# Kernel tuning notes

Hardware: AMD Instinct MI355X
Metric: run time of the kernel (lower is better)

Reference implementation:

```python
import jax, jax.numpy as jnp
from jax import lax
import numpy as np

B, N = 16, 4096
NPOINT, RADIUS, NSAMPLE = 1024, 0.2, 32
IN_CH = 64
MLP = [64, 64, 128]
EPS = 1e-5  # torch BatchNorm2d default


def setup_inputs() -> dict:
    key = jax.random.key(0)
    ks = jax.random.split(key, 2 + 2 * len(MLP))
    inp = {
        "xyz": jax.random.uniform(ks[0], (B, 3, N), jnp.float32),
        "points": jax.random.normal(ks[1], (B, IN_CH, N), jnp.float32),
    }
    last = IN_CH + 3
    for i, out in enumerate(MLP):
        inp[f"W{i}"] = jax.random.normal(ks[2 + 2 * i], (last, out), jnp.float32) / np.float32(np.sqrt(last))
        inp[f"b{i}"] = jnp.zeros((out,), jnp.float32)
        inp[f"g{i}"] = jnp.ones((out,), jnp.float32)
        inp[f"be{i}"] = jnp.zeros((out,), jnp.float32)
        last = out
    return inp


def _fps(x):
    """Farthest point sampling. x: [B,N,3] -> [B,NPOINT] int32 (start idx 0)."""
    Bv, Nn, _ = x.shape

    def step(carry, _):
        dist, far = carry
        c = jnp.take_along_axis(x, far[:, None, None], axis=1)  # [B,1,3]
        d = jnp.sum((x - c) ** 2, axis=-1)                      # [B,N]
        dist = jnp.minimum(dist, d)
        return (dist, jnp.argmax(dist, axis=-1).astype(jnp.int32)), far

    init = (jnp.full((Bv, Nn), 1e10, x.dtype), jnp.zeros((Bv,), jnp.int32))
    _, cent = lax.scan(step, init, None, length=NPOINT)
    return cent.T  # [B, NPOINT]


def _ball_query(x, new_xyz):
    """x: [B,N,3], new_xyz: [B,S,3] -> idx [B,S,NSAMPLE] int32."""
    Nn = x.shape[1]
    sqr = jnp.sum((new_xyz[:, :, None, :] - x[:, None, :, :]) ** 2, axis=-1)  # [B,S,N]
    idx = jnp.where(sqr > RADIUS ** 2, Nn, jnp.arange(Nn, dtype=jnp.int32))
    idx = jnp.sort(idx, axis=-1)[:, :, :NSAMPLE]  # first NSAMPLE in-radius indices
    first = idx[:, :, :1]
    return jnp.where(idx == Nn, first, idx)


def _gather(pts, idx):
    """pts: [B,N,C], idx: [B,S,K] -> [B,S,K,C]."""
    Bv, S, K = idx.shape
    flat = idx.reshape(Bv, S * K)
    return jnp.take_along_axis(pts, flat[:, :, None], axis=1).reshape(Bv, S, K, pts.shape[-1])


def _forward(xyz, points, params):
    x = xyz.transpose(0, 2, 1)      # [B,N,3]
    p = points.transpose(0, 2, 1)   # [B,N,D]
    fps_idx = _fps(x)
    new_xyz = jnp.take_along_axis(x, fps_idx[:, :, None], axis=1)  # [B,S,3]
    idx = _ball_query(x, new_xyz)
    g_xyz = _gather(x, idx) - new_xyz[:, :, None, :]               # [B,S,K,3]
    feats = jnp.concatenate([g_xyz, _gather(p, idx)], axis=-1)     # [B,S,K,3+D]
    for (W, b, g, be) in params:
        feats = jnp.einsum('bskc,cd->bskd', feats, W) + b          # 1x1 conv
        mean = feats.mean(axis=(0, 1, 2))                          # BN train-mode batch stats
        var = feats.var(axis=(0, 1, 2))
        feats = jax.nn.relu(g * (feats - mean) * lax.rsqrt(var + EPS) + be)
    new_points = feats.max(axis=2).transpose(0, 2, 1)              # max over nsample -> [B,C',S]
    return new_xyz.transpose(0, 2, 1), new_points


def reference(xyz, points, W0, b0, g0, be0, W1, b1, g1, be1, W2, b2, g2, be2):
    params = [(W0, b0, g0, be0), (W1, b1, g1, be1), (W2, b2, g2, be2)]
    return _forward(xyz, points, params)
```

## Files before the change

### kernel.cpp

```cpp
#include <hip/hip_runtime.h>
#include <hip/hip_bf16.h>
#include <cstdint>


typedef __attribute__((ext_vector_type(8))) short bf16x8;
typedef __attribute__((ext_vector_type(4))) float f32x4;

#define LDA 104

__device__ __forceinline__ unsigned short f2bf(float f) {
  unsigned x = __float_as_uint(f);
  unsigned r = (x + 0x7FFFu + ((x >> 16) & 1u)) >> 16;
  return (unsigned short)r;
}
__device__ __forceinline__ float bf2f(unsigned short u) {
  return __uint_as_float(((unsigned)u) << 16);
}

template <int CTRL>
__device__ __forceinline__ unsigned long long dppmax(unsigned long long k) {
  int lo = (int)(unsigned)k;
  int hi = (int)(unsigned)(k >> 32);
  int plo = __builtin_amdgcn_update_dpp(lo, lo, CTRL, 0xF, 0xF, false);
  int phi = __builtin_amdgcn_update_dpp(hi, hi, CTRL, 0xF, 0xF, false);
  unsigned long long o =
      ((unsigned long long)(unsigned)phi << 32) | (unsigned)plo;
  return (o > k) ? o : k;
}

__global__ __attribute__((amdgpu_flat_work_group_size(256, 256),
                          amdgpu_waves_per_eu(1, 1)))
void fps_prep_kernel(
    const float* __restrict__ xyz, const float* __restrict__ points,
    const float* __restrict__ W0, const float* __restrict__ W1,
    const float* __restrict__ W2, unsigned short* __restrict__ pT,
    unsigned short* __restrict__ w0t, unsigned short* __restrict__ w1t,
    unsigned short* __restrict__ w2t, float* __restrict__ stats_all,
    float* __restrict__ out, float4* __restrict__ centers4)
{
  __shared__ __align__(16) char smraw[61568];
  int tid = threadIdx.x;
  if (blockIdx.x >= 16) {
    int pb = blockIdx.x - 16;
    if (pb < 1024) {
      float (*tile)[65] = (float (*)[65])smraw;
      int b = pb >> 6;
      int n0 = (pb & 63) << 6;
      const float* pbp = points + ((size_t)b << 18);
      for (int i = tid; i < 4096; i += 256) {
        int cc = i >> 6, nn = i & 63;
        tile[cc][nn] = pbp[((size_t)cc << 12) + n0 + nn];
      }
      __syncthreads();
      for (int i = tid; i < 4096; i += 256) {
        int nn = i >> 6, cc = i & 63;
        pT[(((size_t)((b << 12) + n0 + nn)) << 6) + cc] = f2bf(tile[cc][nn]);
      }
    } else {
      for (int i = tid; i < 27136; i += 256) {
        if (i < 6656) {
          int nn = i / 104, kk = i % 104;
          float v = (kk < 64) ? W0[(3 + kk) * 64 + nn]
                              : ((kk < 67) ? W0[(kk - 64) * 64 + nn] : 0.f);
          w0t[i] = f2bf(v);
        } else if (i < 13312) {
          int j = i - 6656; int nn = j / 104, kk = j % 104;
          float v = (kk < 64) ? W1[kk * 64 + nn] : 0.f;
          w1t[j] = f2bf(v);
        } else if (i < 26624) {
          int j = i - 13312; int nn = j / 104, kk = j % 104;
          float v = (kk < 64) ? W2[kk * 128 + nn] : 0.f;
          w2t[j] = f2bf(v);
        } else {
          stats_all[i - 26624] = 0.f;
        }
      }
    }
    return;
  }
  float* xs  = (float*)smraw;
  float* ys  = xs + 4096;
  float* zs  = ys + 4096;
  float* cxl = zs + 4096;
  float* cyl = cxl + 1024;
  float* czl = cyl + 1024;
  unsigned long long (*keybuf)[4] =
      (unsigned long long (*)[4])(smraw + 61440);

  int b = blockIdx.x;
  const float* xb = xyz + (size_t)b * 12288;
  float px[16], py[16], pz[16], dist[16];
#pragma unroll
  for (int j = 0; j < 16; ++j) {
    int n = tid + (j << 8);
    px[j] = xb[n]; py[j] = xb[4096 + n]; pz[j] = xb[8192 + n];
    xs[n] = px[j]; ys[n] = py[j]; zs[n] = pz[j];
    dist[j] = 1e10f;
  }
  __syncthreads();
  float cx = xs[0], cy = ys[0], cz = zs[0];
  if (tid == 0) { cxl[0] = cx; cyl[0] = cy; czl[0] = cz; }
  int w = tid >> 6;
  int lane = tid & 63;
  for (int it = 1; it < 1024; ++it) {
    float bv = -1.f; int bi = 0;
#pragma unroll
    for (int j = 0; j < 16; ++j) {
      float dx = __fsub_rn(px[j], cx);
      float dy = __fsub_rn(py[j], cy);
      float dz = __fsub_rn(pz[j], cz);
      float d  = __fadd_rn(__fadd_rn(__fmul_rn(dx, dx), __fmul_rn(dy, dy)),
                           __fmul_rn(dz, dz));
      float nd = fminf(dist[j], d);
      dist[j] = nd;
      if (nd > bv) { bv = nd; bi = tid + (j << 8); }
    }
    unsigned long long k =
        ((unsigned long long)__float_as_uint(bv) << 32) | (unsigned)(~bi);
    k = dppmax<0xB1>(k);
    k = dppmax<0x4E>(k);
    k = dppmax<0x141>(k);
    k = dppmax<0x140>(k);
    k = dppmax<0x142>(k);
    k = dppmax<0x143>(k);
    int p = it & 1;
    if (lane == 63) keybuf[p][w] = k;
    __syncthreads();
    uint4 ka2 = *(const uint4*)&keybuf[p][0];
    uint4 kb2 = *(const uint4*)&keybuf[p][2];
    unsigned long long k0 = ((unsigned long long)ka2.y << 32) | ka2.x;
    unsigned long long k1 = ((unsigned long long)ka2.w << 32) | ka2.z;
    unsigned long long k2 = ((unsigned long long)kb2.y << 32) | kb2.x;
    unsigned long long k3 = ((unsigned long long)kb2.w << 32) | kb2.z;
    unsigned long long m01 = (k1 > k0) ? k1 : k0;
    unsigned long long m23 = (k3 > k2) ? k3 : k2;
    unsigned long long km  = (m23 > m01) ? m23 : m01;
    int gi = (int)(~(unsigned)km) & 4095;
    cx = xs[gi]; cy = ys[gi]; cz = zs[gi];
    if (tid == 0) { cxl[it] = cx; cyl[it] = cy; czl[it] = cz; }
  }
  __syncthreads();
  for (int it = tid; it < 1024; it += 256) {
    float x = cxl[it], y = cyl[it], z = czl[it];
    out[b * 3072 + it]        = x;
    out[b * 3072 + 1024 + it] = y;
    out[b * 3072 + 2048 + it] = z;
    centers4[(b << 10) + it]  = make_float4(x, y, z, 0.f);
  }
}

__global__ __launch_bounds__(256) void ball_kernel(const float* __restrict__ xyz,
                                                   const float4* __restrict__ centers4,
                                                   int* __restrict__ ballidx)
{
  __shared__ float xs[4096], ys[4096], zs[4096];
  int tid = threadIdx.x;
  int b = blockIdx.x >> 4;
  int g = blockIdx.x & 15;
  const float* xb = xyz + (size_t)b * 12288;
  for (int i = tid; i < 4096; i += 256) {
    xs[i] = xb[i]; ys[i] = xb[4096 + i]; zs[i] = xb[8192 + i];
  }
  __syncthreads();
  int w = tid >> 6, lane = tid & 63;
  unsigned long long lmask = (1ull << lane) - 1ull;
  for (int j = 0; j < 16; ++j) {
    int s = (g << 6) + (j << 2) + w;
    float4 c = centers4[(b << 10) + s];
    int* ob = ballidx + (((size_t)((b << 10) + s)) << 5);
    int cnt = 0, first = 0;
    for (int m = 0; m < 64; ++m) {
      int n = (m << 6) + lane;
      float dx = __fsub_rn(xs[n], c.x);
      float dy = __fsub_rn(ys[n], c.y);
      float dz = __fsub_rn(zs[n], c.z);
      float d  = __fadd_rn(__fadd_rn(__fmul_rn(dx, dx), __fmul_rn(dy, dy)),
                           __fmul_rn(dz, dz));
      bool hit = !(d > 0.04f);
      unsigned long long mask = __ballot(hit);
      if (cnt == 0 && mask != 0ull)
        first = (m << 6) + (__ffsll((long long)mask) - 1);
      int p = cnt + (int)__popcll(mask & lmask);
      if (hit && p < 32) ob[p] = n;
      cnt += (int)__popcll(mask);
      if (cnt >= 32) break;
    }
    if (lane < 32 && lane >= cnt) ob[lane] = first;
  }
}

__global__ __launch_bounds__(256) void gemm1_kernel(
    const float* __restrict__ xyz, const unsigned short* __restrict__ pT,
    const unsigned short* __restrict__ w0t, const float* __restrict__ b0,
    const float4* __restrict__ centers4, const int* __restrict__ ballidx,
    unsigned short* __restrict__ feats1, float* __restrict__ partials)
{
  __shared__ unsigned short As[64 * LDA];
  __shared__ unsigned short Wt[64 * LDA];
  __shared__ float red[2][4][64];
  int tid = threadIdx.x;
  int blockbase = blockIdx.x << 8;
  int b = blockbase >> 15;
  {
    const uint4* wsrc = (const uint4*)w0t;
    uint4* wdst = (uint4*)Wt;
    for (int i = tid; i < 832; i += 256) wdst[i] = wsrc[i];
  }
  int lane = tid & 63, w = tid >> 6;
  int mrow = (w << 4) + (lane & 15);
  int quad = lane >> 4;
  float a0acc = 0.f, a1acc = 0.f;
  for (int t = 0; t < 4; ++t) {
    int rowbase = blockbase + (t << 6);
    {
      int rl = tid >> 2, part = tid & 3;
      int r = rowbase + rl;
      int n = ballidx[r];
      const uint4* psrc = (const uint4*)(pT + (((size_t)((b << 12) + n)) << 6));
      uint4* adst = (uint4*)(As + rl * LDA);
      adst[part * 2]     = psrc[part * 2];
      adst[part * 2 + 1] = psrc[part * 2 + 1];
      adst[8 + part] = make_uint4(0, 0, 0, 0);
      if (part == 0) {
        int ci = r >> 5;
        float4 c = centers4[ci];
        unsigned short* arow = As + rl * LDA;
        arow[64] = f2bf(__fsub_rn(xyz[(size_t)b * 12288 + n],        c.x));
        arow[65] = f2bf(__fsub_rn(xyz[(size_t)b * 12288 + 4096 + n], c.y));
        arow[66] = f2bf(__fsub_rn(xyz[(size_t)b * 12288 + 8192 + n], c.z));
      }
    }
    __syncthreads();
    f32x4 acc[4];
#pragma unroll
    for (int nt = 0; nt < 4; ++nt) acc[nt] = (f32x4){0.f, 0.f, 0.f, 0.f};
#pragma unroll
    for (int kt = 0; kt < 3; ++kt) {
      int ko = kt * 32 + (quad << 3);
      bf16x8 a = *(const bf16x8*)(As + mrow * LDA + ko);
#pragma unroll
      for (int nt = 0; nt < 4; ++nt) {
        bf16x8 bb = *(const bf16x8*)(Wt + ((nt << 4) + (lane & 15)) * LDA + ko);
        acc[nt] = __builtin_amdgcn_mfma_f32_16x16x32_bf16(a, bb, acc[nt], 0, 0, 0);
      }
    }
#pragma unroll
    for (int nt = 0; nt < 4; ++nt) {
      int cch = (nt << 4) + (lane & 15);
      float bias = b0[cch];
      float ssum = 0.f, sq = 0.f;
#pragma unroll
      for (int r2 = 0; r2 < 4; ++r2) {
        float y = acc[nt][r2] + bias;
        int ml = (w << 4) + (quad << 2) + r2;
        feats1[(((size_t)(rowbase + ml)) << 6) + cch] = f2bf(y);
        ssum += y; sq += y * y;
      }
      ssum += __shfl_xor(ssum, 16); ssum += __shfl_xor(ssum, 32);
      sq   += __shfl_xor(sq, 16);   sq   += __shfl_xor(sq, 32);
      if (quad == 0) { red[0][w][cch] = ssum; red[1][w][cch] = sq; }
    }
    __syncthreads();
    if (tid < 64) {
      a0acc += red[0][0][tid] + red[0][1][tid] + red[0][2][tid] + red[0][3][tid];
      a1acc += red[1][0][tid] + red[1][1][tid] + red[1][2][tid] + red[1][3][tid];
    }
  }
  if (tid < 64) {
    partials[(size_t)blockIdx.x * 256 + tid]      = a0acc;
    partials[(size_t)blockIdx.x * 256 + 64 + tid] = a1acc;
  }
}

__global__ __launch_bounds__(256) void gemm2_kernel(
    const unsigned short* __restrict__ featsIn, const unsigned short* __restrict__ wt,
    const float* __restrict__ bias_g, const float* __restrict__ ss_in,
    unsigned short* __restrict__ featsOut, float* __restrict__ partials)
{
  __shared__ unsigned short As[64 * LDA];
  __shared__ unsigned short Wt[64 * LDA];
  __shared__ float red[2][4][64];
  __shared__ float ssl[128];
  int tid = threadIdx.x;
  int blockbase = blockIdx.x << 8;
  if (tid < 128) ssl[tid] = ss_in[tid];
  {
    const uint4* wsrc = (const uint4*)wt;
    uint4* wdst = (uint4*)Wt;
    for (int i = tid; i < 832; i += 256) wdst[i] = wsrc[i];
  }
  int lane = tid & 63, w = tid >> 6;
  int mrow = (w << 4) + (lane & 15);
  int quad = lane >> 4;
  float a0acc = 0.f, a1acc = 0.f;
  __syncthreads();
  for (int t = 0; t < 4; ++t) {
    int rowbase = blockbase + (t << 6);
    {
      int rl = tid >> 2, part = tid & 3;
      size_t r = (size_t)rowbase + rl;
      union { uint4 v[2]; unsigned short u[16]; } tt;
      const uint4* src = (const uint4*)(featsIn + (r << 6));
      tt.v[0] = src[part * 2]; tt.v[1] = src[part * 2 + 1];
      union { uint4 v[2]; unsigned short u[16]; } o;
#pragma unroll
      for (int e = 0; e < 16; ++e) {
        int cch = (part << 4) + e;
        float f = bf2f(tt.u[e]);
        float y = fmaxf(f * ssl[cch] + ssl[64 + cch], 0.f);
        o.u[e] = f2bf(y);
      }
      uint4* adst = (uint4*)(As + rl * LDA + (part << 4));
      adst[0] = o.v[0]; adst[1] = o.v[1];
    }
    __syncthreads();
    f32x4 acc[4];
#pragma unroll
    for (int nt = 0; nt < 4; ++nt) acc[nt] = (f32x4){0.f, 0.f, 0.f, 0.f};
#pragma unroll
    for (int kt = 0; kt < 2; ++kt) {
      int ko = kt * 32 + (quad << 3);
      bf16x8 a = *(const bf16x8*)(As + mrow * LDA + ko);
#pragma unroll
      for (int nt = 0; nt < 4; ++nt) {
        bf16x8 bb = *(const bf16x8*)(Wt + ((nt << 4) + (lane & 15)) * LDA + ko);
        acc[nt] = __builtin_amdgcn_mfma_f32_16x16x32_bf16(a, bb, acc[nt], 0, 0, 0);
      }
    }
#pragma unroll
    for (int nt = 0; nt < 4; ++nt) {
      int cch = (nt << 4) + (lane & 15);
      float bias = bias_g[cch];
      float ssum = 0.f, sq = 0.f;
#pragma unroll
      for (int r2 = 0; r2 < 4; ++r2) {
        float y = acc[nt][r2] + bias;
        int ml = (w << 4) + (quad << 2) + r2;
        featsOut[(((size_t)(rowbase + ml)) << 6) + cch] = f2bf(y);
        ssum += y; sq += y * y;
      }
      ssum += __shfl_xor(ssum, 16); ssum += __shfl_xor(ssum, 32);
      sq   += __shfl_xor(sq, 16);   sq   += __shfl_xor(sq, 32);
      if (quad == 0) { red[0][w][cch] = ssum; red[1][w][cch] = sq; }
    }
    __syncthreads();
    if (tid < 64) {
      a0acc += red[0][0][tid] + red[0][1][tid] + red[0][2][tid] + red[0][3][tid];
      a1acc += red[1][0][tid] + red[1][1][tid] + red[1][2][tid] + red[1][3][tid];
    }
  }
  if (tid < 64) {
    partials[(size_t)blockIdx.x * 256 + tid]      = a0acc;
    partials[(size_t)blockIdx.x * 256 + 64 + tid] = a1acc;
  }
}

__global__ __launch_bounds__(256) void gemm3_stats_kernel(
    const unsigned short* __restrict__ feats2, const unsigned short* __restrict__ w2t,
    const float* __restrict__ b2, const float* __restrict__ ss2,
    float* __restrict__ partials, float* __restrict__ y3mx,
    float* __restrict__ y3mn)
{
  __shared__ unsigned short As[64 * LDA];
  __shared__ unsigned short Wt[128 * LDA];
  __shared__ float red[2][4][128];
  __shared__ float mxw[4][128];
  __shared__ float mnw[4][128];
  __shared__ float ssl[128];
  int tid = threadIdx.x;
  int blockbase = blockIdx.x << 8;
  if (tid < 128) ssl[tid] = ss2[tid];
  {
    const uint4* wsrc = (const uint4*)w2t;
    uint4* wdst = (uint4*)Wt;
    for (int i = tid; i < 1664; i += 256) wdst[i] = wsrc[i];
  }
  int lane = tid & 63, w = tid >> 6;
  int mrow = (w << 4) + (lane & 15);
  int quad = lane >> 4;
  float a0acc = 0.f, a1acc = 0.f;
  __syncthreads();
  for (int t = 0; t < 4; ++t) {
    int rowbase = blockbase + (t << 6);
    {
      int rl = tid >> 2, part = tid & 3;
      size_t r = (size_t)rowbase + rl;
      union { uint4 v[2]; unsigned short u[16]; } tt;
      const uint4* src = (const uint4*)(feats2 + (r << 6));
      tt.v[0] = src[part * 2]; tt.v[1] = src[part * 2 + 1];
      union { uint4 v[2]; unsigned short u[16]; } o;
#pragma unroll
      for (int e = 0; e < 16; ++e) {
        int cch = (part << 4) + e;
        float f = bf2f(tt.u[e]);
        float y = fmaxf(f * ssl[cch] + ssl[64 + cch], 0.f);
        o.u[e] = f2bf(y);
      }
      uint4* adst = (uint4*)(As + rl * LDA + (part << 4));
      adst[0] = o.v[0]; adst[1] = o.v[1];
    }
    __syncthreads();
    f32x4 acc[8];
#pragma unroll
    for (int nt = 0; nt < 8; ++nt) acc[nt] = (f32x4){0.f, 0.f, 0.f, 0.f};
#pragma unroll
    for (int kt = 0; kt < 2; ++kt) {
      int ko = kt * 32 + (quad << 3);
      bf16x8 a = *(const bf16x8*)(As + mrow * LDA + ko);
#pragma unroll
      for (int nt = 0; nt < 8; ++nt) {
        bf16x8 bb = *(const bf16x8*)(Wt + ((nt << 4) + (lane & 15)) * LDA + ko);
        acc[nt] = __builtin_amdgcn_mfma_f32_16x16x32_bf16(a, bb, acc[nt], 0, 0, 0);
      }
    }
#pragma unroll
    for (int nt = 0; nt < 8; ++nt) {
      int cch = (nt << 4) + (lane & 15);
      float bias = b2[cch];
      float ssum = 0.f, sq = 0.f;
      float mx = -3.4e38f, mn = 3.4e38f;
#pragma unroll
      for (int r2 = 0; r2 < 4; ++r2) {
        float y = acc[nt][r2] + bias;
        ssum += y; sq += y * y;
        mx = fmaxf(mx, y); mn = fminf(mn, y);
      }
      ssum += __shfl_xor(ssum, 16); ssum += __shfl_xor(ssum, 32);
      sq   += __shfl_xor(sq, 16);   sq   += __shfl_xor(sq, 32);
      mx = fmaxf(mx, __shfl_xor(mx, 16)); mx = fmaxf(mx, __shfl_xor(mx, 32));
      mn = fminf(mn, __shfl_xor(mn, 16)); mn = fminf(mn, __shfl_xor(mn, 32));
      if (quad == 0) {
        red[0][w][cch] = ssum; red[1][w][cch] = sq;
        mxw[w][cch] = mx; mnw[w][cch] = mn;
      }
    }
    __syncthreads();
    if (tid < 128) {
      a0acc += red[0][0][tid] + red[0][1][tid] + red[0][2][tid] + red[0][3][tid];
      a1acc += red[1][0][tid] + red[1][1][tid] + red[1][2][tid] + red[1][3][tid];
    }
    {
      int c2 = tid >> 7, cch = tid & 127;
      int cg = (rowbase >> 5) + c2;
      y3mx[((size_t)cg << 7) + cch] = fmaxf(mxw[2 * c2][cch], mxw[2 * c2 + 1][cch]);
      y3mn[((size_t)cg << 7) + cch] = fminf(mnw[2 * c2][cch], mnw[2 * c2 + 1][cch]);
    }
  }
  if (tid < 128) {
    partials[(size_t)blockIdx.x * 256 + tid]       = a0acc;
    partials[(size_t)blockIdx.x * 256 + 128 + tid] = a1acc;
  }
}

__global__ __launch_bounds__(256) void reduce_kernel(const float* __restrict__ partials,
                                                     float* __restrict__ stats, int twoC)
{
  int tid = threadIdx.x;
  if (tid < twoC) {
    int row0 = blockIdx.x << 5;
    float s = 0.f;
    for (int r = 0; r < 32; ++r) s += partials[((size_t)(row0 + r)) * 256 + tid];
    atomicAdd(&stats[tid], s);
  }
}

__global__ void finalize_kernel(const float* __restrict__ stats, const float* __restrict__ g,
                                const float* __restrict__ be, float* __restrict__ ss, int C)
{
  int c = threadIdx.x;
  if (c < C) {
    const float invM = 1.f / 524288.f;
    float mean = stats[c] * invM;
    float ex2  = stats[C + c] * invM;
    float var  = ex2 - mean * mean;
    float sc   = g[c] / sqrtf(var + 1e-5f);
    ss[c]     = sc;
    ss[C + c] = be[c] - mean * sc;
  }
}

__global__ __launch_bounds__(256) void bn3_out_kernel(
    const float* __restrict__ y3mx, const float* __restrict__ y3mn,
    const float* __restrict__ ss3, float* __restrict__ out)
{
  __shared__ float t2[64][65];
  __shared__ float sl[128];
  int tid = threadIdx.x;
  int b = blockIdx.x >> 5;
  int rest = blockIdx.x & 31;
  int s0 = (rest & 15) << 6;
  int c0 = (rest >> 4) << 6;
  if (tid < 64) sl[tid] = ss3[c0 + tid];
  else if (tid < 128) sl[tid] = ss3[128 + c0 + (tid - 64)];
  __syncthreads();
  for (int i = tid; i < 4096; i += 256) {
    int row = i >> 6, col = i & 63;
    size_t cg = (size_t)((b << 10) + s0 + row);
    float mx = y3mx[(cg << 7) + c0 + col];
    float mn = y3mn[(cg << 7) + c0 + col];
    float sc = sl[col], sh = sl[64 + col];
    float ye = (sc >= 0.f) ? mx : mn;
    t2[row][col] = fmaxf(ye * sc + sh, 0.f);
  }
  __syncthreads();
  for (int i = tid; i < 4096; i += 256) {
    int crow = i >> 6, scol = i & 63;
    out[49152 + ((size_t)b << 17) + (size_t)(c0 + crow) * 1024 + s0 + scol] = t2[scol][crow];
  }
}

extern "C" void kernel_launch(void* const* d_in, const int* in_sizes, int n_in,
                              void* d_out, int out_size, void* d_ws, size_t ws_size,
                              hipStream_t stream)
{
  (void)in_sizes; (void)n_in; (void)out_size; (void)ws_size;
  const float* xyz    = (const float*)d_in[0];
  const float* points = (const float*)d_in[1];
  const float* W0  = (const float*)d_in[2];
  const float* b0  = (const float*)d_in[3];
  const float* g0  = (const float*)d_in[4];
  const float* be0 = (const float*)d_in[5];
  const float* W1  = (const float*)d_in[6];
  const float* b1  = (const float*)d_in[7];
  const float* g1  = (const float*)d_in[8];
  const float* be1 = (const float*)d_in[9];
  const float* W2  = (const float*)d_in[10];
  const float* b2  = (const float*)d_in[11];
  const float* g2  = (const float*)d_in[12];
  const float* be2 = (const float*)d_in[13];
  float* out = (float*)d_out;

  char* base = (char*)d_ws;
  size_t off = 0;
  auto alloc = [&](size_t bytes) -> void* {
    void* p = base + off;
    off += (bytes + 255) & ~(size_t)255;
    return p;
  };
  unsigned short* pT     = (unsigned short*)alloc((size_t)16 * 4096 * 64 * 2);
  unsigned short* w0t    = (unsigned short*)alloc(64 * LDA * 2);
  unsigned short* w1t    = (unsigned short*)alloc(64 * LDA * 2);
  unsigned short* w2t    = (unsigned short*)alloc(128 * LDA * 2);
  float* stats_all       = (float*)alloc(512 * 4);
  float* ss_all          = (float*)alloc(512 * 4);
  float4* centers4       = (float4*)alloc((size_t)16 * 1024 * 16);
  int* ballidx           = (int*)alloc((size_t)16 * 1024 * 32 * 4);
  unsigned short* feats1 = (unsigned short*)alloc((size_t)524288 * 64 * 2);
  unsigned short* feats2 = (unsigned short*)alloc((size_t)524288 * 64 * 2);
  float* partials        = (float*)alloc((size_t)2048 * 256 * 4);

  float* y3mx = (float*)feats1;
  float* y3mn = y3mx + (size_t)16384 * 128;

  float* stats1 = stats_all;       float* stats2 = stats_all + 128; float* stats3 = stats_all + 256;
  float* ss1 = ss_all;             float* ss2 = ss_all + 128;       float* ss3 = ss_all + 256;

  fps_prep_kernel<<<1041, 256, 0, stream>>>(xyz, points, W0, W1, W2, pT, w0t, w1t,
                                            w2t, stats_all, out, centers4);
  ball_kernel<<<256, 256, 0, stream>>>(xyz, centers4, ballidx);
  gemm1_kernel<<<2048, 256, 0, stream>>>(xyz, pT, w0t, b0, centers4, ballidx, feats1, partials);
  reduce_kernel<<<64, 256, 0, stream>>>(partials, stats1, 128);
  finalize_kernel<<<1, 64, 0, stream>>>(stats1, g0, be0, ss1, 64);
  gemm2_kernel<<<2048, 256, 0, stream>>>(feats1, w1t, b1, ss1, feats2, partials);
  reduce_kernel<<<64, 256, 0, stream>>>(partials, stats2, 128);
  finalize_kernel<<<1, 64, 0, stream>>>(stats2, g1, be1, ss2, 64);
  gemm3_stats_kernel<<<2048, 256, 0, stream>>>(feats2, w2t, b2, ss2, partials, y3mx, y3mn);
  reduce_kernel<<<64, 256, 0, stream>>>(partials, stats3, 256);
  finalize_kernel<<<1, 128, 0, stream>>>(stats3, g2, be2, ss3, 128);
  bn3_out_kernel<<<512, 256, 0, stream>>>(y3mx, y3mn, ss3, out);
}
```

Before: 914.1 us.

## Fuse FPS, prep, ball query and GEMM1 into persistent cooperative kernel

```diff
diff --git a/kernel.cpp b/kernel.cpp
--- a/kernel.cpp
+++ b/kernel.cpp
@@ -28,247 +28,291 @@
   return (o > k) ? o : k;
 }
 
+__device__ __forceinline__ void spin_ge(int* p, int need) {
+  while (__hip_atomic_load(p, __ATOMIC_ACQUIRE, __HIP_MEMORY_SCOPE_AGENT) < need)
+    __builtin_amdgcn_s_sleep(32);
+}
+
 __global__ __attribute__((amdgpu_flat_work_group_size(256, 256),
                           amdgpu_waves_per_eu(1, 1)))
-void fps_prep_kernel(
+void mega_kernel(
     const float* __restrict__ xyz, const float* __restrict__ points,
     const float* __restrict__ W0, const float* __restrict__ W1,
-    const float* __restrict__ W2, unsigned short* __restrict__ pT,
-    unsigned short* __restrict__ w0t, unsigned short* __restrict__ w1t,
-    unsigned short* __restrict__ w2t, float* __restrict__ stats_all,
-    float* __restrict__ out, float4* __restrict__ centers4)
+    const float* __restrict__ W2, const float* __restrict__ b0,
+    unsigned short* __restrict__ pT, unsigned short* __restrict__ w0t,
+    unsigned short* __restrict__ w1t, unsigned short* __restrict__ w2t,
+    float4* __restrict__ centers4, unsigned short* __restrict__ feats1,
+    float* __restrict__ partials, float* __restrict__ out,
+    int* __restrict__ ctrl)
 {
   __shared__ __align__(16) char smraw[61568];
+  __shared__ int tkt_s;
   int tid = threadIdx.x;
-  if (blockIdx.x >= 16) {
-    int pb = blockIdx.x - 16;
-    if (pb < 1024) {
-      float (*tile)[65] = (float (*)[65])smraw;
-      int b = pb >> 6;
-      int n0 = (pb & 63) << 6;
-      const float* pbp = points + ((size_t)b << 18);
-      for (int i = tid; i < 4096; i += 256) {
-        int cc = i >> 6, nn = i & 63;
-        tile[cc][nn] = pbp[((size_t)cc << 12) + n0 + nn];
-      }
+  int bx = blockIdx.x;
+  int* progress  = ctrl;
+  int* prep_done = ctrl + 16;
+  int* g1_ticket = ctrl + 17;
+
+  if (bx < 16) {
+    float* xs  = (float*)smraw;
+    float* ys  = xs + 4096;
+    float* zs  = ys + 4096;
+    float* cxl = zs + 4096;
+    float* cyl = cxl + 1024;
+    float* czl = cyl + 1024;
+    unsigned long long (*keybuf)[4] =
+        (unsigned long long (*)[4])(smraw + 61440);
+
+    int b = bx;
+    const float* xb = xyz + (size_t)b * 12288;
+    float px[16], py[16], pz[16], dist[16];
+#pragma unroll
+    for (int j = 0; j < 16; ++j) {
+      int n = tid + (j << 8);
+      px[j] = xb[n]; py[j] = xb[4096 + n]; pz[j] = xb[8192 + n];
+      xs[n] = px[j]; ys[n] = py[j]; zs[n] = pz[j];
+      dist[j] = 1e10f;
+    }
+    __syncthreads();
+    float cx = xs[0], cy = ys[0], cz = zs[0];
+    if (tid == 0) { cxl[0] = cx; cyl[0] = cy; czl[0] = cz; }
+    int w = tid >> 6;
+    int lane = tid & 63;
+    for (int it = 1; it < 1024; ++it) {
+      float bv = -1.f; int bi = 0;
+#pragma unroll
+      for (int j = 0; j < 16; ++j) {
+        float dx = __fsub_rn(px[j], cx);
+        float dy = __fsub_rn(py[j], cy);
+        float dz = __fsub_rn(pz[j], cz);
+        float d  = __fadd_rn(__fadd_rn(__fmul_rn(dx, dx), __fmul_rn(dy, dy)),
+                             __fmul_rn(dz, dz));
+        float nd = fminf(dist[j], d);
+        dist[j] = nd;
+        if (nd > bv) { bv = nd; bi = tid + (j << 8); }
+      }
+      unsigned long long k =
+          ((unsigned long long)__float_as_uint(bv) << 32) | (unsigned)(~bi);
+      k = dppmax<0xB1>(k);
+      k = dppmax<0x4E>(k);
+      k = dppmax<0x141>(k);
+      k = dppmax<0x140>(k);
+      k = dppmax<0x142>(k);
+      k = dppmax<0x143>(k);
+      int p = it & 1;
+      if (lane == 63) keybuf[p][w] = k;
       __syncthreads();
-      for (int i = tid; i < 4096; i += 256) {
-        int nn = i >> 6, cc = i & 63;
-        pT[(((size_t)((b << 12) + n0 + nn)) << 6) + cc] = f2bf(tile[cc][nn]);
-      }
-    } else {
-      for (int i = tid; i < 27136; i += 256) {
-        if (i < 6656) {
-          int nn = i / 104, kk = i % 104;
-          float v = (kk < 64) ? W0[(3 + kk) * 64 + nn]
-                              : ((kk < 67) ? W0[(kk - 64) * 64 + nn] : 0.f);
-          w0t[i] = f2bf(v);
-        } else if (i < 13312) {
-          int j = i - 6656; int nn = j / 104, kk = j % 104;
-          float v = (kk < 64) ? W1[kk * 64 + nn] : 0.f;
-          w1t[j] = f2bf(v);
-        } else if (i < 26624) {
-          int j = i - 13312; int nn = j / 104, kk = j % 104;
-          float v = (kk < 64) ? W2[kk * 128 + nn] : 0.f;
-          w2t[j] = f2bf(v);
-        } else {
-          stats_all[i - 26624] = 0.f;
-        }
-      }
-    }
-    return;
-  }
-  float* xs  = (float*)smraw;
-  float* ys  = xs + 4096;
-  float* zs  = ys + 4096;
-  float* cxl = zs + 4096;
-  float* cyl = cxl + 1024;
-  float* czl = cyl + 1024;
-  unsigned long long (*keybuf)[4] =
-      (unsigned long long (*)[4])(smraw + 61440);
-
-  int b = blockIdx.x;
-  const float* xb = xyz + (size_t)b * 12288;
-  float px[16], py[16], pz[16], dist[16];
-#pragma unroll
-  for (int j = 0; j < 16; ++j) {
-    int n = tid + (j << 8);
-    px[j] = xb[n]; py[j] = xb[4096 + n]; pz[j] = xb[8192 + n];
-    xs[n] = px[j]; ys[n] = py[j]; zs[n] = pz[j];
-    dist[j] = 1e10f;
-  }
+      uint4 ka2 = *(const uint4*)&keybuf[p][0];
+      uint4 kb2 = *(const uint4*)&keybuf[p][2];
+      unsigned long long k0 = ((unsigned long long)ka2.y << 32) | ka2.x;
+      unsigned long long k1 = ((unsigned long long)ka2.w << 32) | ka2.z;
+      unsigned long long k2 = ((unsigned long long)kb2.y << 32) | kb2.x;
+      unsigned long long k3 = ((unsigned long long)kb2.w << 32) | kb2.z;
+      unsigned long long m01 = (k1 > k0) ? k1 : k0;
+      unsigned long long m23 = (k3 > k2) ? k3 : k2;
+      unsigned long long km  = (m23 > m01) ? m23 : m01;
+      int gi = (int)(~(unsigned)km) & 4095;
+      cx = xs[gi]; cy = ys[gi]; cz = zs[gi];
+      if (tid == 0) { cxl[it] = cx; cyl[it] = cy; czl[it] = cz; }
+      if ((it & 63) == 0) {
+        int base = it - 64;
+        if (tid < 64) {
+          int s = base + tid;
+          centers4[(b << 10) + s] = make_float4(cxl[s], cyl[s], czl[s], 0.f);
+        }
+        if (tid == 0) {
+          __threadfence();
+          __hip_atomic_store(&progress[b], it, __ATOMIC_RELEASE,
+                             __HIP_MEMORY_SCOPE_AGENT);
+        }
+      }
+    }
+    __syncthreads();
+    for (int it = tid; it < 1024; it += 256) {
+      float x = cxl[it], y = cyl[it], z = czl[it];
+      out[b * 3072 + it]        = x;
+      out[b * 3072 + 1024 + it] = y;
+      out[b * 3072 + 2048 + it] = z;
+      centers4[(b << 10) + it]  = make_float4(x, y, z, 0.f);
+    }
+    __syncthreads();
+    if (tid == 0) {
+      __threadfence();
+      __hip_atomic_store(&progress[b], 1024, __ATOMIC_RELEASE,
+                         __HIP_MEMORY_SCOPE_AGENT);
+    }
+  } else {
+    int wid = bx - 16;
+    int cnt = 0;
+    for (int t = wid; t < 1025; t += 240) {
+      __syncthreads();
+      if (t < 1024) {
+        float (*tile)[65] = (float (*)[65])smraw;
+        int b = t >> 6;
+        int n0 = (t & 63) << 6;
+        const float* pbp = points + ((size_t)b << 18);
+        for (int i = tid; i < 4096; i += 256) {
+          int cc = i >> 6, nn = i & 63;
+          tile[cc][nn] = pbp[((size_t)cc << 12) + n0 + nn];
+        }
+        __syncthreads();
+        for (int i = tid; i < 4096; i += 256) {
+          int nn = i >> 6, cc = i & 63;
+          pT[(((size_t)((b << 12) + n0 + nn)) << 6) + cc] = f2bf(tile[cc][nn]);
+        }
+      } else {
+        for (int i = tid; i < 26624; i += 256) {
+          if (i < 6656) {
+            int nn = i / 104, kk = i % 104;
+            float v = (kk < 64) ? W0[(3 + kk) * 64 + nn]
+                                : ((kk < 67) ? W0[(kk - 64) * 64 + nn] : 0.f);
+            w0t[i] = f2bf(v);
+          } else if (i < 13312) {
+            int j = i - 6656; int nn = j / 104, kk = j % 104;
+            w1t[j] = f2bf((kk < 64) ? W1[kk * 64 + nn] : 0.f);
+          } else {
+            int j = i - 13312; int nn = j / 104, kk = j % 104;
+            w2t[j] = f2bf((kk < 64) ? W2[kk * 128 + nn] : 0.f);
+          }
+        }
+      }
+      ++cnt;
+    }
+    __syncthreads();
+    if (tid == 0) {
+      __threadfence();
+      __hip_atomic_fetch_add(prep_done, cnt, __ATOMIC_RELEASE,
+                             __HIP_MEMORY_SCOPE_AGENT);
+    }
+  }
+
+  spin_ge(prep_done, 1025);
   __syncthreads();
-  float cx = xs[0], cy = ys[0], cz = zs[0];
-  if (tid == 0) { cxl[0] = cx; cyl[0] = cy; czl[0] = cz; }
-  int w = tid >> 6;
-  int lane = tid & 63;
-  for (int it = 1; it < 1024; ++it) {
-    float bv = -1.f; int bi = 0;
-#pragma unroll
-    for (int j = 0; j < 16; ++j) {
-      float dx = __fsub_rn(px[j], cx);
-      float dy = __fsub_rn(py[j], cy);
-      float dz = __fsub_rn(pz[j], cz);
-      float d  = __fadd_rn(__fadd_rn(__fmul_rn(dx, dx), __fmul_rn(dy, dy)),
-                           __fmul_rn(dz, dz));
-      float nd = fminf(dist[j], d);
-      dist[j] = nd;
-      if (nd > bv) { bv = nd; bi = tid + (j << 8); }
-    }
-    unsigned long long k =
-        ((unsigned long long)__float_as_uint(bv) << 32) | (unsigned)(~bi);
-    k = dppmax<0xB1>(k);
-    k = dppmax<0x4E>(k);
-    k = dppmax<0x141>(k);
-    k = dppmax<0x140>(k);
-    k = dppmax<0x142>(k);
-    k = dppmax<0x143>(k);
-    int p = it & 1;
-    if (lane == 63) keybuf[p][w] = k;
-    __syncthreads();
-    uint4 ka2 = *(const uint4*)&keybuf[p][0];
-    uint4 kb2 = *(const uint4*)&keybuf[p][2];
-    unsigned long long k0 = ((unsigned long long)ka2.y << 32) | ka2.x;
-    unsigned long long k1 = ((unsigned long long)ka2.w << 32) | ka2.z;
-    unsigned long long k2 = ((unsigned long long)kb2.y << 32) | kb2.x;
-    unsigned long long k3 = ((unsigned long long)kb2.w << 32) | kb2.z;
-    unsigned long long m01 = (k1 > k0) ? k1 : k0;
-    unsigned long long m23 = (k3 > k2) ? k3 : k2;
-    unsigned long long km  = (m23 > m01) ? m23 : m01;
-    int gi = (int)(~(unsigned)km) & 4095;
-    cx = xs[gi]; cy = ys[gi]; cz = zs[gi];
-    if (tid == 0) { cxl[it] = cx; cyl[it] = cy; czl[it] = cz; }
-  }
-  __syncthreads();
-  for (int it = tid; it < 1024; it += 256) {
-    float x = cxl[it], y = cyl[it], z = czl[it];
-    out[b * 3072 + it]        = x;
-    out[b * 3072 + 1024 + it] = y;
-    out[b * 3072 + 2048 + it] = z;
-    centers4[(b << 10) + it]  = make_float4(x, y, z, 0.f);
-  }
-}
-
-__global__ __launch_bounds__(256) void ball_kernel(const float* __restrict__ xyz,
-                                                   const float4* __restrict__ centers4,
-                                                   int* __restrict__ ballidx)
-{
-  __shared__ float xs[4096], ys[4096], zs[4096];
-  int tid = threadIdx.x;
-  int b = blockIdx.x >> 4;
-  int g = blockIdx.x & 15;
-  const float* xb = xyz + (size_t)b * 12288;
-  for (int i = tid; i < 4096; i += 256) {
-    xs[i] = xb[i]; ys[i] = xb[4096 + i]; zs[i] = xb[8192 + i];
-  }
-  __syncthreads();
-  int w = tid >> 6, lane = tid & 63;
-  unsigned long long lmask = (1ull << lane) - 1ull;
-  for (int j = 0; j < 16; ++j) {
-    int s = (g << 6) + (j << 2) + w;
-    float4 c = centers4[(b << 10) + s];
-    int* ob = ballidx + (((size_t)((b << 10) + s)) << 5);
-    int cnt = 0, first = 0;
-    for (int m = 0; m < 64; ++m) {
-      int n = (m << 6) + lane;
-      float dx = __fsub_rn(xs[n], c.x);
-      float dy = __fsub_rn(ys[n], c.y);
-      float dz = __fsub_rn(zs[n], c.z);
-      float d  = __fadd_rn(__fadd_rn(__fmul_rn(dx, dx), __fmul_rn(dy, dy)),
-                           __fmul_rn(dz, dz));
-      bool hit = !(d > 0.04f);
-      unsigned long long mask = __ballot(hit);
-      if (cnt == 0 && mask != 0ull)
-        first = (m << 6) + (__ffsll((long long)mask) - 1);
-      int p = cnt + (int)__popcll(mask & lmask);
-      if (hit && p < 32) ob[p] = n;
-      cnt += (int)__popcll(mask);
-      if (cnt >= 32) break;
-    }
-    if (lane < 32 && lane >= cnt) ob[lane] = first;
-  }
-}
-
-__global__ __launch_bounds__(256) void gemm1_kernel(
-    const float* __restrict__ xyz, const unsigned short* __restrict__ pT,
-    const unsigned short* __restrict__ w0t, const float* __restrict__ b0,
-    const float4* __restrict__ centers4, const int* __restrict__ ballidx,
-    unsigned short* __restrict__ feats1, float* __restrict__ partials)
-{
-  __shared__ unsigned short As[64 * LDA];
-  __shared__ unsigned short Wt[64 * LDA];
-  __shared__ float red[2][4][64];
-  int tid = threadIdx.x;
-  int blockbase = blockIdx.x << 8;
-  int b = blockbase >> 15;
-  {
-    const uint4* wsrc = (const uint4*)w0t;
-    uint4* wdst = (uint4*)Wt;
-    for (int i = tid; i < 832; i += 256) wdst[i] = wsrc[i];
-  }
+
+  float* xs = (float*)smraw;
+  float* ys = xs + 4096;
+  float* zs = ys + 4096;
+  unsigned short* As = (unsigned short*)smraw;
+  unsigned short* Wt = (unsigned short*)(smraw + 13312);
+  float* red = (float*)(smraw + 26624);
+  int* idxl = (int*)(smraw + 60416);
+
   int lane = tid & 63, w = tid >> 6;
   int mrow = (w << 4) + (lane & 15);
   int quad = lane >> 4;
-  float a0acc = 0.f, a1acc = 0.f;
-  for (int t = 0; t < 4; ++t) {
-    int rowbase = blockbase + (t << 6);
+  unsigned long long lmask = (1ull << lane) - 1ull;
+
+  for (;;) {
+    if (tid == 0) tkt_s = atomicAdd(g1_ticket, 1);
+    __syncthreads();
+    int tk = tkt_s;
+    if (tk >= 2048) break;
+    int tile = ((tk & 15) << 7) | (tk >> 4);
+    int b = tile >> 7;
+    int s0 = (tile & 127) << 3;
+    spin_ge(&progress[b], s0 + 8);
+
     {
-      int rl = tid >> 2, part = tid & 3;
-      int r = rowbase + rl;
-      int n = ballidx[r];
-      const uint4* psrc = (const uint4*)(pT + (((size_t)((b << 12) + n)) << 6));
-      uint4* adst = (uint4*)(As + rl * LDA);
-      adst[part * 2]     = psrc[part * 2];
-      adst[part * 2 + 1] = psrc[part * 2 + 1];
-      adst[8 + part] = make_uint4(0, 0, 0, 0);
-      if (part == 0) {
-        int ci = r >> 5;
-        float4 c = centers4[ci];
-        unsigned short* arow = As + rl * LDA;
-        arow[64] = f2bf(__fsub_rn(xyz[(size_t)b * 12288 + n],        c.x));
-        arow[65] = f2bf(__fsub_rn(xyz[(size_t)b * 12288 + 4096 + n], c.y));
-        arow[66] = f2bf(__fsub_rn(xyz[(size_t)b * 12288 + 8192 + n], c.z));
-      }
-    }
-    __syncthreads();
-    f32x4 acc[4];
-#pragma unroll
-    for (int nt = 0; nt < 4; ++nt) acc[nt] = (f32x4){0.f, 0.f, 0.f, 0.f};
-#pragma unroll
-    for (int kt = 0; kt < 3; ++kt) {
-      int ko = kt * 32 + (quad << 3);
-      bf16x8 a = *(const bf16x8*)(As + mrow * LDA + ko);
+      const float* xb = xyz + (size_t)b * 12288;
+      for (int i = tid; i < 4096; i += 256) {
+        xs[i] = xb[i]; ys[i] = xb[4096 + i]; zs[i] = xb[8192 + i];
+      }
+    }
+    __syncthreads();
+    {
+      int cg0 = (b << 10) + s0;
+      for (int c2 = 0; c2 < 2; ++c2) {
+        int sl = (w << 1) + c2;
+        float4 c = centers4[cg0 + sl];
+        int* ob = idxl + (sl << 5);
+        int cnt2 = 0, first = 0;
+        for (int m = 0; m < 64; ++m) {
+          int n = (m << 6) + lane;
+          float dx = __fsub_rn(xs[n], c.x);
+          float dy = __fsub_rn(ys[n], c.y);
+          float dz = __fsub_rn(zs[n], c.z);
+          float d  = __fadd_rn(__fadd_rn(__fmul_rn(dx, dx), __fmul_rn(dy, dy)),
+                               __fmul_rn(dz, dz));
+          bool hit = !(d > 0.04f);
+          unsigned long long mask = __ballot(hit);
+          if (cnt2 == 0 && mask != 0ull)
+            first = (m << 6) + (__ffsll((long long)mask) - 1);
+          int p = cnt2 + (int)__popcll(mask & lmask);
+          if (hit && p < 32) ob[p] = n;
+          cnt2 += (int)__popcll(mask);
+          if (cnt2 >= 32) break;
+        }
+        if (lane < 32 && lane >= cnt2) ob[lane] = first;
+      }
+    }
+    __syncthreads();
+
+    {
+      const uint4* wsrc = (const uint4*)w0t;
+      uint4* wdst = (uint4*)Wt;
+      for (int i = tid; i < 832; i += 256) wdst[i] = wsrc[i];
+    }
+    float a0acc = 0.f, a1acc = 0.f;
+    for (int tt = 0; tt < 4; ++tt) {
+      int rowbase = (tile << 8) + (tt << 6);
+      {
+        int rl = tid >> 2, part = tid & 3;
+        int n = idxl[(tt << 6) + rl];
+        const uint4* psrc = (const uint4*)(pT + (((size_t)((b << 12) + n)) << 6));
+        uint4* adst = (uint4*)(As + rl * LDA);
+        adst[part * 2]     = psrc[part * 2];
+        adst[part * 2 + 1] = psrc[part * 2 + 1];
+        adst[8 + part] = make_uint4(0, 0, 0, 0);
+        if (part == 0) {
+          int r = rowbase + rl;
+          float4 c = centers4[r >> 5];
+          unsigned short* arow = As + rl * LDA;
+          arow[64] = f2bf(__fsub_rn(xyz[(size_t)b * 12288 + n],        c.x));
+          arow[65] = f2bf(__fsub_rn(xyz[(size_t)b * 12288 + 4096 + n], c.y));
+          arow[66] = f2bf(__fsub_rn(xyz[(size_t)b * 12288 + 8192 + n], c.z));
+        }
+      }
+      __syncthreads();
+      f32x4 acc[4];
+#pragma unroll
+      for (int nt = 0; nt < 4; ++nt) acc[nt] = (f32x4){0.f, 0.f, 0.f, 0.f};
+#pragma unroll
+      for (int kt = 0; kt < 3; ++kt) {
+        int ko = kt * 32 + (quad << 3);
+        bf16x8 a = *(const bf16x8*)(As + mrow * LDA + ko);
+#pragma unroll
+        for (int nt = 0; nt < 4; ++nt) {
+          bf16x8 bb = *(const bf16x8*)(Wt + ((nt << 4) + (lane & 15)) * LDA + ko);
+          acc[nt] = __builtin_amdgcn_mfma_f32_16x16x32_bf16(a, bb, acc[nt], 0, 0, 0);
+        }
+      }
 #pragma unroll
       for (int nt = 0; nt < 4; ++nt) {
-        bf16x8 bb = *(const bf16x8*)(Wt + ((nt << 4) + (lane & 15)) * LDA + ko);
-        acc[nt] = __builtin_amdgcn_mfma_f32_16x16x32_bf16(a, bb, acc[nt], 0, 0, 0);
-      }
-    }
-#pragma unroll
-    for (int nt = 0; nt < 4; ++nt) {
-      int cch = (nt << 4) + (lane & 15);
-      float bias = b0[cch];
-      float ssum = 0.f, sq = 0.f;
-#pragma unroll
-      for (int r2 = 0; r2 < 4; ++r2) {
-        float y = acc[nt][r2] + bias;
-        int ml = (w << 4) + (quad << 2) + r2;
-        feats1[(((size_t)(rowbase + ml)) << 6) + cch] = f2bf(y);
-        ssum += y; sq += y * y;
-      }
-      ssum += __shfl_xor(ssum, 16); ssum += __shfl_xor(ssum, 32);
-      sq   += __shfl_xor(sq, 16);   sq   += __shfl_xor(sq, 32);
-      if (quad == 0) { red[0][w][cch] = ssum; red[1][w][cch] = sq; }
-    }
-    __syncthreads();
+        int cch = (nt << 4) + (lane & 15);
+        float bias = b0[cch];
+        float ssum = 0.f, sq = 0.f;
+#pragma unroll
+        for (int r2 = 0; r2 < 4; ++r2) {
+          float y = acc[nt][r2] + bias;
+          int ml = (w << 4) + (quad << 2) + r2;
+          feats1[(((size_t)(rowbase + ml)) << 6) + cch] = f2bf(y);
+          ssum += y; sq += y * y;
+        }
+        ssum += __shfl_xor(ssum, 16); ssum += __shfl_xor(ssum, 32);
+        sq   += __shfl_xor(sq, 16);   sq   += __shfl_xor(sq, 32);
+        if (quad == 0) { red[w * 64 + cch] = ssum; red[256 + w * 64 + cch] = sq; }
+      }
+      __syncthreads();
+      if (tid < 64) {
+        a0acc += red[tid] + red[64 + tid] + red[128 + tid] + red[192 + tid];
+        a1acc += red[256 + tid] + red[320 + tid] + red[384 + tid] + red[448 + tid];
+      }
+    }
     if (tid < 64) {
-      a0acc += red[0][0][tid] + red[0][1][tid] + red[0][2][tid] + red[0][3][tid];
-      a1acc += red[1][0][tid] + red[1][1][tid] + red[1][2][tid] + red[1][3][tid];
-    }
-  }
-  if (tid < 64) {
-    partials[(size_t)blockIdx.x * 256 + tid]      = a0acc;
-    partials[(size_t)blockIdx.x * 256 + 64 + tid] = a1acc;
+      partials[(size_t)tile * 256 + tid]      = a0acc;
+      partials[(size_t)tile * 256 + 64 + tid] = a1acc;
+    }
+    __syncthreads();
   }
 }
 
@@ -544,10 +588,10 @@
   float* stats_all       = (float*)alloc(512 * 4);
   float* ss_all          = (float*)alloc(512 * 4);
   float4* centers4       = (float4*)alloc((size_t)16 * 1024 * 16);
-  int* ballidx           = (int*)alloc((size_t)16 * 1024 * 32 * 4);
   unsigned short* feats1 = (unsigned short*)alloc((size_t)524288 * 64 * 2);
   unsigned short* feats2 = (unsigned short*)alloc((size_t)524288 * 64 * 2);
   float* partials        = (float*)alloc((size_t)2048 * 256 * 4);
+  int* ctrl              = (int*)alloc(4096);
 
   float* y3mx = (float*)feats1;
   float* y3mn = y3mx + (size_t)16384 * 128;
@@ -555,10 +599,21 @@
   float* stats1 = stats_all;       float* stats2 = stats_all + 128; float* stats3 = stats_all + 256;
   float* ss1 = ss_all;             float* ss2 = ss_all + 128;       float* ss3 = ss_all + 256;
 
-  fps_prep_kernel<<<1041, 256, 0, stream>>>(xyz, points, W0, W1, W2, pT, w0t, w1t,
-                                            w2t, stats_all, out, centers4);
-  ball_kernel<<<256, 256, 0, stream>>>(xyz, centers4, ballidx);
-  gemm1_kernel<<<2048, 256, 0, stream>>>(xyz, pT, w0t, b0, centers4, ballidx, feats1, partials);
+  hipMemsetAsync(ctrl, 0, 4096, stream);
+  hipMemsetAsync(stats_all, 0, 512 * 4, stream);
+
+  void* kargs[15] = {
+    (void*)&xyz, (void*)&points, (void*)&W0, (void*)&W1, (void*)&W2,
+    (void*)&b0, (void*)&pT, (void*)&w0t, (void*)&w1t, (void*)&w2t,
+    (void*)&centers4, (void*)&feats1, (void*)&partials, (void*)&out,
+    (void*)&ctrl
+  };
+  if (hipLaunchCooperativeKernel((void*)mega_kernel, dim3(256), dim3(256),
+                                 kargs, 0, stream) != hipSuccess) {
+    mega_kernel<<<256, 256, 0, stream>>>(xyz, points, W0, W1, W2, b0, pT, w0t,
+                                         w1t, w2t, centers4, feats1, partials,
+                                         out, ctrl);
+  }
   reduce_kernel<<<64, 256, 0, stream>>>(partials, stats1, 128);
   finalize_kernel<<<1, 64, 0, stream>>>(stats1, g0, be0, ss1, 64);
   gemm2_kernel<<<2048, 256, 0, stream>>>(feats1, w1t, b1, ss1, feats2, partials);
```

Result: no change. 919.3 us (+0.6%).
